# Optimization experiments

Measured on AMD Instinct MI355X. Metric: run time of the kernel, lower is better.

## Reference

```python
import jax, jax.numpy as jnp
import numpy as np

B, N, M = 2, 10000, 320000
F, LAT, STY = 64, 128, 128
HEADS, HID = 4, 32
OUT = 3 + F  # 67
NEG = 0.2    # leaky relu slope (both activation and GAT attention)
EPS = 1e-5


def leaky(x):
    return jax.nn.leaky_relu(x, NEG)


def layer_norm(x, g, b):
    mu = jnp.mean(x, axis=-1, keepdims=True)
    var = jnp.var(x, axis=-1, keepdims=True)
    return (x - mu) * jax.lax.rsqrt(var + EPS) * g + b


def gat_conv(h, src, dst, W, a_src, a_dst, bias, heads, out_dim, n_nodes, concat):
    # h: [n, in]; W: [in, heads*out_dim]; a_*: [heads, out_dim]
    ht = (h @ W).reshape(n_nodes, heads, out_dim)
    al_s = jnp.einsum('nhd,hd->nh', ht, a_src)  # source contribution
    al_d = jnp.einsum('nhd,hd->nh', ht, a_dst)  # destination contribution
    e = leaky(al_s[src] + al_d[dst])            # [E, heads]
    emax = jax.ops.segment_max(e, dst, num_segments=n_nodes)
    ex = jnp.exp(e - emax[dst])
    denom = jax.ops.segment_sum(ex, dst, num_segments=n_nodes)
    alpha = ex / (denom[dst] + 1e-16)           # scatter-softmax over in-edges
    msg = ht[src] * alpha[:, :, None]           # [E, heads, out_dim]
    agg = jax.ops.segment_sum(msg, dst, num_segments=n_nodes)
    agg = agg.reshape(n_nodes, heads * out_dim) if concat else agg.mean(axis=1)
    return agg + bias


def setup_inputs():
    key = jax.random.key(0)
    ks = jax.random.split(key, 20)
    g = lambda i, sh, s=0.05: jax.random.normal(ks[i], sh, jnp.float32) * s
    d = {}
    d['z'] = g(0, (B, LAT), 1.0)
    d['x'] = g(1, (N, F), 1.0)
    d['pos'] = g(2, (N, 3), 1.0)
    d['edge_index'] = jax.random.randint(ks[3], (2, M), 0, N)
    d['w1'] = g(4, (LAT, 256)); d['b1'] = jnp.zeros((256,), jnp.float32)
    d['w2'] = g(5, (256, 512)); d['b2'] = jnp.zeros((512,), jnp.float32)
    d['w3'] = g(6, (512, STY)); d['b3'] = jnp.zeros((STY,), jnp.float32)
    in0 = F + STY
    d['gw0'] = g(7, (in0, HEADS * HID)); d['ga0s'] = g(8, (HEADS, HID)); d['ga0d'] = g(9, (HEADS, HID)); d['gb0'] = jnp.zeros((HEADS * HID,), jnp.float32)
    in1 = HEADS * HID
    d['gw1'] = g(10, (in1, HEADS * HID)); d['ga1s'] = g(11, (HEADS, HID)); d['ga1d'] = g(12, (HEADS, HID)); d['gb1'] = jnp.zeros((HEADS * HID,), jnp.float32)
    d['gw2'] = g(13, (in1, OUT)); d['ga2s'] = g(14, (1, OUT)); d['ga2d'] = g(15, (1, OUT)); d['gb2'] = jnp.zeros((OUT,), jnp.float32)
    d['ln0_g'] = jnp.ones((in1,), jnp.float32); d['ln0_b'] = jnp.zeros((in1,), jnp.float32)
    d['ln1_g'] = jnp.ones((in1,), jnp.float32); d['ln1_b'] = jnp.zeros((in1,), jnp.float32)
    return d


def _batched_edges(edge_index):
    # replicate template edges B times with node-id offsets, then add self-loops
    ei = jnp.concatenate([edge_index + b * N for b in range(B)], axis=1)
    sl = jnp.arange(B * N, dtype=edge_index.dtype)
    src = jnp.concatenate([ei[0], sl])
    dst = jnp.concatenate([ei[1], sl])
    return src, dst


def _forward(z, x, pos, src, dst,
             w1, b1, w2, b2, w3, b3,
             gw0, ga0s, ga0d, gb0, gw1, ga1s, ga1d, gb1, gw2, ga2s, ga2d, gb2,
             ln0_g, ln0_b, ln1_g, ln1_b):
    n_tot = B * N
    # style MLP
    s = leaky(z @ w1 + b1)
    s = leaky(s @ w2 + b2)
    style = s @ w3 + b3                               # [B, STY]
    xb = jnp.tile(x, (B, 1))                          # [B*N, F]
    pb = jnp.tile(pos, (B, 1))                        # [B*N, 3]
    style_exp = jnp.repeat(style, N, axis=0)          # [B*N, STY]
    H = jnp.concatenate([xb, style_exp], axis=1)
    H = gat_conv(H, src, dst, gw0, ga0s, ga0d, gb0, HEADS, HID, n_tot, True)
    H = leaky(layer_norm(H, ln0_g, ln0_b))
    H = gat_conv(H, src, dst, gw1, ga1s, ga1d, gb1, HEADS, HID, n_tot, True)
    H = leaky(layer_norm(H, ln1_g, ln1_b))
    H_out = gat_conv(H, src, dst, gw2, ga2s, ga2d, gb2, 1, OUT, n_tot, False)
    p_new = pb + H_out[:, :3]
    f_new = xb + H_out[:, 3:]
    return f_new, p_new


def reference(z, x, pos, edge_index,
              w1, b1, w2, b2, w3, b3,
              gw0, ga0s, ga0d, gb0, gw1, ga1s, ga1d, gb1, gw2, ga2s, ga2d, gb2,
              ln0_g, ln0_b, ln1_g, ln1_b):
    src, dst = _batched_edges(edge_index)
    return _forward(z, x, pos, src, dst,
                    w1, b1, w2, b2, w3, b3,
                    gw0, ga0s, ga0d, gb0, gw1, ga1s, ga1d, gb1, gw2, ga2s, ga2d, gb2,
                    ln0_g, ln0_b, ln1_g, ln1_b)
```

## Files before the change

### kernel.cpp

```cpp
#include <hip/hip_runtime.h>
#include <hip/hip_bf16.h>

#define DEV_INLINE __device__ __forceinline__

constexpr int Nn   = 10000;
constexpr int NT   = 20000;
constexpr int Me   = 320000;
constexpr int STRIDE = 96;
constexpr float NEG = 0.2f;

typedef float  f32x4  __attribute__((ext_vector_type(4)));
typedef short  bf16x8 __attribute__((ext_vector_type(8)));

DEV_INLINE float leaky(float x){ return x >= 0.f ? x : NEG*x; }

DEV_INLINE ushort f2bf(float v){
  __hip_bfloat16 h = __float2bfloat16(v);
  return *reinterpret_cast<ushort*>(&h);
}
DEV_INLINE float bf2f(ushort u){
  uint x = ((uint)u) << 16;
  return __uint_as_float(x);
}
DEV_INLINE float sel4(float4 w, int h){
  return h < 2 ? (h == 0 ? w.x : w.y) : (h == 2 ? w.z : w.w);
}
DEV_INLINE float red16(float v){
  v += __shfl_xor(v, 1); v += __shfl_xor(v, 2);
  v += __shfl_xor(v, 4); v += __shfl_xor(v, 8);
  return v;
}
DEV_INLINE float red32(float v){
  v += __shfl_xor(v, 1); v += __shfl_xor(v, 2);
  v += __shfl_xor(v, 4); v += __shfl_xor(v, 8);
  v += __shfl_xor(v, 16);
  return v;
}

template<int K>
__global__ __launch_bounds__(256) void k_mlp(const float* __restrict__ in,
    const float* __restrict__ W, const float* __restrict__ bias,
    float* __restrict__ out, int OD, int doAct, int mlpBlocks,
    int* __restrict__ zbuf, int zn){
  if ((int)blockIdx.x >= mlpBlocks){
    int i = (blockIdx.x - mlpBlocks)*256 + threadIdx.x;
    if (i < zn) zbuf[i] = 0;
    return;
  }
  int wave = threadIdx.x >> 6, lane = threadIdx.x & 63;
  int o = blockIdx.x*4 + wave;
  if (o >= 2*OD) return;
  int b = (o >= OD) ? 1 : 0;
  int j = o - b*OD;
  const float* __restrict__ ip = in + b*K;
  float acc = 0.f;
  #pragma unroll 2
  for (int k = lane; k < K; k += 64) acc += ip[k] * W[(size_t)k*OD + j];
  #pragma unroll
  for (int off = 32; off; off >>= 1) acc += __shfl_xor(acc, off);
  if (lane == 0){
    float v = acc + (bias ? bias[j] : 0.f);
    out[o] = doAct ? leaky(v) : v;
  }
}

__global__ __launch_bounds__(256) void k_ht0(const float* __restrict__ x,
    const float* __restrict__ gw0, const float* __restrict__ styleW0,
    const float* __restrict__ a_s, const float* __restrict__ a_d,
    ushort* __restrict__ ht0, float* __restrict__ alS, float* __restrict__ alD){
  __shared__ float wl[64][128];
  __shared__ float xl[32][64];
  __shared__ float sw[2][128];
  __shared__ float stycS[2][4], stycD[2][4];
  int t = threadIdx.x;
  for (int i=t; i<64*128; i+=256) wl[i>>7][i&127] = gw0[i];
  if (t < 256) sw[t>>7][t&127] = styleW0[t];
  int row0 = blockIdx.x*32;
  for (int i=t; i<32*64; i+=256){
    int r = i>>6, c = i&63; int gr = row0 + r;
    xl[r][c] = (gr < Nn) ? x[gr*64 + c] : 0.f;
  }
  __syncthreads();
  int c = t & 127, rh = t >> 7, lane = t & 63;
  float as_c = a_s[c], ad_c = a_d[c];
  int h = c >> 5;

  if (t < 128){
    float v0s = sw[0][c]*as_c, v0d = sw[0][c]*ad_c;
    float v1s = sw[1][c]*as_c, v1d = sw[1][c]*ad_c;
    v0s = red32(v0s); v0d = red32(v0d);
    v1s = red32(v1s); v1d = red32(v1d);
    if ((lane & 31) == 0){
      stycS[0][h] = v0s; stycD[0][h] = v0d;
      stycS[1][h] = v1s; stycD[1][h] = v1d;
    }
  }

  float acc[16];
  #pragma unroll
  for (int i=0;i<16;i++) acc[i]=0.f;
  for (int k=0;k<64;k++){
    float w = wl[k][c];
    #pragma unroll
    for (int i=0;i<16;i++) acc[i] += xl[rh+2*i][k]*w;
  }
  __syncthreads();
  float s0 = sw[0][c], s1 = sw[1][c];
  #pragma unroll
  for (int i=0;i<16;i++){
    int gr = row0 + rh + 2*i;
    if (gr < Nn){
      ht0[(size_t)gr*128 + c]      = f2bf(acc[i] + s0);
      ht0[(size_t)(Nn+gr)*128 + c] = f2bf(acc[i] + s1);
    }
    float vs = acc[i]*as_c, vd = acc[i]*ad_c;
    vs = red32(vs); vd = red32(vd);
    if ((lane & 31) == 0 && gr < Nn){
      alS[(size_t)gr*4 + h]      = vs + stycS[0][h];
      alD[(size_t)gr*4 + h]      = vd + stycD[0][h];
      alS[(size_t)(Nn+gr)*4 + h] = vs + stycS[1][h];
      alD[(size_t)(Nn+gr)*4 + h] = vd + stycD[1][h];
    }
  }
}

template<int NCOL, int LDO, int NF, int NHEAD>
__global__ __launch_bounds__(256) void k_mm_mfma(const ushort* __restrict__ A,
    const float* __restrict__ W, ushort* __restrict__ out,
    const float* __restrict__ a_s, const float* __restrict__ a_d,
    float* __restrict__ alS, float* __restrict__ alD, int M){
  constexpr int NCOLP = NF*16;
  __shared__ ushort bt[NCOLP*128];
  int t = threadIdx.x;
  int wid = t >> 6, lane = t & 63, l15 = lane & 15, g = lane >> 4;
  int mbase = blockIdx.x*128 + wid*32;

  bf16x8 afr[2][4];
  #pragma unroll
  for (int mf=0; mf<2; mf++){
    int row = mbase + mf*16 + l15;
    int rc = row < M ? row : M-1;
    const ushort* ap = A + (size_t)rc*128 + g*8;
    #pragma unroll
    for (int ks=0; ks<4; ks++)
      afr[mf][ks] = *(const bf16x8*)(ap + ks*32);
  }

  for (int idx = t; idx < 128*NCOLP; idx += 256){
    int k = idx / NCOLP, c = idx % NCOLP;
    float v = (c < NCOL) ? W[k*NCOL + c] : 0.f;
    uint byte = ((uint)(c*128 + k) << 1) ^ ((uint)(c&7) << 4);
    *(ushort*)((char*)bt + byte) = f2bf(v);
  }
  __syncthreads();

  f32x4 acc[2][NF];
  #pragma unroll
  for (int mf=0; mf<2; mf++)
    #pragma unroll
    for (int nf=0; nf<NF; nf++) acc[mf][nf] = (f32x4){0.f,0.f,0.f,0.f};

  #pragma unroll
  for (int ks=0; ks<4; ks++){
    int kb = ks*32 + g*8;
    bf16x8 bfr[NF];
    #pragma unroll
    for (int nf=0; nf<NF; nf++){
      int c = nf*16 + l15;
      uint byte = ((uint)(c*128 + kb) << 1) ^ ((uint)(c&7) << 4);
      bfr[nf] = *(const bf16x8*)((const char*)bt + byte);
    }
    #pragma unroll
    for (int mf=0; mf<2; mf++)
      #pragma unroll
      for (int nf=0; nf<NF; nf++)
        acc[mf][nf] = __builtin_amdgcn_mfma_f32_16x16x32_bf16(
            afr[mf][ks], bfr[nf], acc[mf][nf], 0, 0, 0);
  }

  #pragma unroll
  for (int mf=0; mf<2; mf++){
    int rbase = mbase + mf*16 + g*4;
    #pragma unroll
    for (int nf=0; nf<NF; nf++){
      int c = nf*16 + l15;
      if (c < LDO){
        #pragma unroll
        for (int r=0; r<4; r++){
          int row = rbase + r;
          if (row < M) out[(size_t)row*LDO + c] = (c < NCOL) ? f2bf(acc[mf][nf][r]) : (ushort)0;
        }
      }
    }
  }

  float as_v[NF], ad_v[NF];
  #pragma unroll
  for (int nf=0; nf<NF; nf++){
    int c = nf*16 + l15;
    as_v[nf] = (c < NCOL) ? a_s[c] : 0.f;
    ad_v[nf] = (c < NCOL) ? a_d[c] : 0.f;
  }
  #pragma unroll
  for (int mf=0; mf<2; mf++){
    #pragma unroll
    for (int r=0; r<4; r++){
      int row = mbase + mf*16 + g*4 + r;
      if (NHEAD == 4){
        float ps0 = acc[mf][0][r]*as_v[0] + acc[mf][1][r]*as_v[1];
        float ps1 = acc[mf][2][r]*as_v[2] + acc[mf][3][r]*as_v[3];
        float ps2 = acc[mf][4][r]*as_v[4] + acc[mf][5][r]*as_v[5];
        float ps3 = acc[mf][6][r]*as_v[6] + acc[mf][7][r]*as_v[7];
        float pd0 = acc[mf][0][r]*ad_v[0] + acc[mf][1][r]*ad_v[1];
        float pd1 = acc[mf][2][r]*ad_v[2] + acc[mf][3][r]*ad_v[3];
        float pd2 = acc[mf][4][r]*ad_v[4] + acc[mf][5][r]*ad_v[5];
        float pd3 = acc[mf][6][r]*ad_v[6] + acc[mf][7][r]*ad_v[7];
        ps0 = red16(ps0); ps1 = red16(ps1); ps2 = red16(ps2); ps3 = red16(ps3);
        pd0 = red16(pd0); pd1 = red16(pd1); pd2 = red16(pd2); pd3 = red16(pd3);
        if (l15 == 0 && row < M){
          *(float4*)(alS + (size_t)row*4) = make_float4(ps0, ps1, ps2, ps3);
          *(float4*)(alD + (size_t)row*4) = make_float4(pd0, pd1, pd2, pd3);
        }
      } else {
        float ps = 0.f, pd = 0.f;
        #pragma unroll
        for (int nf=0; nf<NF; nf++){
          ps += acc[mf][nf][r]*as_v[nf];
          pd += acc[mf][nf][r]*ad_v[nf];
        }
        ps = red16(ps); pd = red16(pd);
        if (l15 == 0 && row < M){
          alS[row] = ps; alD[row] = pd;
        }
      }
    }
  }
}

__global__ void k_scatter(const int* __restrict__ eidx,
    int* __restrict__ cnt, ushort* __restrict__ slot){
  int e = blockIdx.x*256 + threadIdx.x;
  if (e >= Me) return;
  int s = eidx[e], d = eidx[Me + e];
  int p = atomicAdd(&cnt[d], 1);
  if (p < STRIDE) slot[(size_t)d*STRIDE + p] = (ushort)s;
}

__global__ __launch_bounds__(256) void k_gat128(const ushort* __restrict__ ht,
    const float* __restrict__ alS, const float* __restrict__ alD,
    const int* __restrict__ deg, const ushort* __restrict__ slot,
    const float* __restrict__ gb, const float* __restrict__ lng,
    const float* __restrict__ lnb, ushort* __restrict__ outH, int n){
  __shared__ float4 wbuf[4][64];
  __shared__ int    sbuf[4][64];
  int wave = threadIdx.x >> 6, lane = threadIdx.x & 63;
  int dd = blockIdx.x*4 + wave;
  if (dd >= n) return;
  int tr  = (dd >= Nn) ? dd - Nn : dd;
  int off = (dd >= Nn) ? Nn : 0;
  int c0 = lane*2;
  int h  = lane >> 4;
  float4 ald4 = *(const float4*)(alD + dd*4);
  int dg = deg[tr]; if (dg > STRIDE) dg = STRIDE;
  int begin = tr*STRIDE, end = begin + dg;

  float4 asl = *(const float4*)(alS + dd*4);
  float4 wsl;
  wsl.x = __expf(leaky(asl.x + ald4.x));
  wsl.y = __expf(leaky(asl.y + ald4.y));
  wsl.z = __expf(leaky(asl.z + ald4.z));
  wsl.w = __expf(leaky(asl.w + ald4.w));
  float es = sel4(wsl, h);
  uint sv0 = *(const uint*)(ht + (size_t)dd*128 + c0);
  float den  = es;
  float acc0 = es * bf2f((ushort)(sv0 & 0xffff));
  float acc1 = es * bf2f((ushort)(sv0 >> 16));

  const ushort* __restrict__ htp = ht + c0;

  for (int j = begin; j < end; j += 64){
    int nc = min(64, end - j);
    if (lane < nc){
      int s = (int)slot[j + lane] + off;
      float4 as4 = *(const float4*)(alS + s*4);
      float4 w;
      w.x = __expf(leaky(as4.x + ald4.x));
      w.y = __expf(leaky(as4.y + ald4.y));
      w.z = __expf(leaky(as4.z + ald4.z));
      w.w = __expf(leaky(as4.w + ald4.w));
      wbuf[wave][lane] = w;
      sbuf[wave][lane] = s;
    }
    int q = 0;
    for (; q + 8 <= nc; q += 8){
      int sv[8]; float4 wv[8];
      #pragma unroll
      for (int u=0;u<8;u++){ sv[u] = sbuf[wave][q+u]; wv[u] = wbuf[wave][q+u]; }
      uint hv[8];
      #pragma unroll
      for (int u=0;u<8;u++) hv[u] = *(const uint*)(htp + (size_t)sv[u]*128);
      #pragma unroll
      for (int u=0;u<8;u++){
        float e = sel4(wv[u], h);
        den  += e;
        acc0 += e * bf2f((ushort)(hv[u] & 0xffff));
        acc1 += e * bf2f((ushort)(hv[u] >> 16));
      }
    }
    for (; q < nc; q++){
      int s = sbuf[wave][q];
      float e = sel4(wbuf[wave][q], h);
      uint hv = *(const uint*)(htp + (size_t)s*128);
      den  += e;
      acc0 += e * bf2f((ushort)(hv & 0xffff));
      acc1 += e * bf2f((ushort)(hv >> 16));
    }
  }
  float idn = 1.f / (den + 1e-16f);
  float v0 = acc0*idn + gb[c0];
  float v1 = acc1*idn + gb[c0+1];

  float sum = v0 + v1, sq = v0*v0 + v1*v1;
  #pragma unroll
  for (int offx = 32; offx; offx >>= 1){
    sum += __shfl_xor(sum, offx);
    sq  += __shfl_xor(sq,  offx);
  }
  float mu  = sum * (1.f/128.f);
  float var = sq  * (1.f/128.f) - mu*mu;
  float inv = rsqrtf(var + 1e-5f);
  float y0 = (v0 - mu)*inv*lng[c0]   + lnb[c0];
  float y1 = (v1 - mu)*inv*lng[c0+1] + lnb[c0+1];
  uint ow = (uint)f2bf(leaky(y0)) | ((uint)f2bf(leaky(y1)) << 16);
  *(uint*)(outH + (size_t)dd*128 + c0) = ow;
}

__global__ __launch_bounds__(256) void k_gat_out(const ushort* __restrict__ ht2,
    const float* __restrict__ alS, const float* __restrict__ alD,
    const int* __restrict__ deg, const ushort* __restrict__ slot,
    const float* __restrict__ gb2, const float* __restrict__ x,
    const float* __restrict__ pos, float* __restrict__ out, int n){
  __shared__ float wbuf[4][64];
  __shared__ int   sbuf[4][64];
  int wave = threadIdx.x >> 6, lane = threadIdx.x & 63;
  int dd = blockIdx.x*4 + wave;
  if (dd >= n) return;
  int tr  = (dd >= Nn) ? dd - Nn : dd;
  int off = (dd >= Nn) ? Nn : 0;
  int c0 = lane*2;
  bool act = (c0 < 67);
  float ald = alD[dd];
  int dg = deg[tr]; if (dg > STRIDE) dg = STRIDE;
  int begin = tr*STRIDE, end = begin + dg;

  float wsl = __expf(leaky(alS[dd] + ald));
  float den  = wsl;
  uint sv0 = act ? *(const uint*)(ht2 + (size_t)dd*68 + c0) : 0u;
  float acc0 = wsl * bf2f((ushort)(sv0 & 0xffff));
  float acc1 = wsl * bf2f((ushort)(sv0 >> 16));

  const ushort* __restrict__ h2p = ht2 + c0;

  for (int j = begin; j < end; j += 64){
    int nc = min(64, end - j);
    if (lane < nc){
      int s = (int)slot[j + lane] + off;
      wbuf[wave][lane] = __expf(leaky(alS[s] + ald));
      sbuf[wave][lane] = s;
    }
    int q = 0;
    for (; q + 8 <= nc; q += 8){
      int sv[8]; float wv[8];
      #pragma unroll
      for (int u=0;u<8;u++){ sv[u] = sbuf[wave][q+u]; wv[u] = wbuf[wave][q+u]; }
      uint hv[8];
      #pragma unroll
      for (int u=0;u<8;u++) hv[u] = act ? *(const uint*)(h2p + (size_t)sv[u]*68) : 0u;
      #pragma unroll
      for (int u=0;u<8;u++){
        den  += wv[u];
        acc0 += wv[u] * bf2f((ushort)(hv[u] & 0xffff));
        acc1 += wv[u] * bf2f((ushort)(hv[u] >> 16));
      }
    }
    for (; q < nc; q++){
      int s = sbuf[wave][q]; float w = wbuf[wave][q];
      uint hv = act ? *(const uint*)(h2p + (size_t)s*68) : 0u;
      den  += w;
      acc0 += w * bf2f((ushort)(hv & 0xffff));
      acc1 += w * bf2f((ushort)(hv >> 16));
    }
  }
  if (!act) return;
  float idn = 1.f / (den + 1e-16f);
  int i = tr;
  int c1 = c0 + 1;
  float v0 = acc0*idn + gb2[c0];
  if (c0 < 3) out[NT*64 + dd*3 + c0] = pos[i*3 + c0] + v0;
  else        out[dd*64 + (c0-3)]    = x[i*64 + (c0-3)] + v0;
  if (c1 < 67){
    float v1 = acc1*idn + gb2[c1];
    if (c1 < 3) out[NT*64 + dd*3 + c1] = pos[i*3 + c1] + v1;
    else        out[dd*64 + (c1-3)]    = x[i*64 + (c1-3)] + v1;
  }
}

extern "C" void kernel_launch(void* const* d_in, const int* in_sizes, int n_in,
                              void* d_out, int out_size, void* d_ws, size_t ws_size,
                              hipStream_t stream){
  const float* z    = (const float*)d_in[0];
  const float* x    = (const float*)d_in[1];
  const float* pos  = (const float*)d_in[2];
  const int*   eidx = (const int*)  d_in[3];
  const float* w1   = (const float*)d_in[4];
  const float* b1   = (const float*)d_in[5];
  const float* w2   = (const float*)d_in[6];
  const float* b2   = (const float*)d_in[7];
  const float* w3   = (const float*)d_in[8];
  const float* b3   = (const float*)d_in[9];
  const float* gw0  = (const float*)d_in[10];
  const float* ga0s = (const float*)d_in[11];
  const float* ga0d = (const float*)d_in[12];
  const float* gb0  = (const float*)d_in[13];
  const float* gw1  = (const float*)d_in[14];
  const float* ga1s = (const float*)d_in[15];
  const float* ga1d = (const float*)d_in[16];
  const float* gb1  = (const float*)d_in[17];
  const float* gw2  = (const float*)d_in[18];
  const float* ga2s = (const float*)d_in[19];
  const float* ga2d = (const float*)d_in[20];
  const float* gb2  = (const float*)d_in[21];
  const float* ln0g = (const float*)d_in[22];
  const float* ln0b = (const float*)d_in[23];
  const float* ln1g = (const float*)d_in[24];
  const float* ln1b = (const float*)d_in[25];
  float* out = (float*)d_out;

  float* ws       = (float*)d_ws;
  float* styleW0  = ws;
  float* s1buf    = ws + 256;
  float* s2buf    = s1buf + 512;
  float* stbuf    = s2buf + 1024;
  float* alS      = stbuf + 256;
  float* alD      = alS + 80000;
  ushort* htA     = (ushort*)(alD + 80000);
  ushort* htB     = htA + (size_t)NT*128;
  ushort* ht2c    = htB + (size_t)NT*128;
  int*   cnt      = (int*)(ht2c + (size_t)NT*68);
  ushort* slot    = (ushort*)(cnt + Nn);

  const int ZB = (Nn + 255)/256;
  k_mlp<128><<<128 + ZB, 256, 0, stream>>>(z,     w1, b1, s1buf, 256, 1, 128, cnt, Nn);
  k_mlp<256><<<256,      256, 0, stream>>>(s1buf, w2, b2, s2buf, 512, 1, 256, nullptr, 0);
  k_mlp<512><<<64,       256, 0, stream>>>(s2buf, w3, b3, stbuf, 128, 0, 64, nullptr, 0);
  k_mlp<128><<<64,       256, 0, stream>>>(stbuf, gw0 + 64*128, (const float*)nullptr, styleW0, 128, 0, 64, nullptr, 0);

  k_scatter<<<(Me+255)/256, 256, 0, stream>>>(eidx, cnt, slot);

  const int MB = (NT+127)/128;
  k_ht0<<<(Nn+31)/32, 256, 0, stream>>>(x, gw0, styleW0, ga0s, ga0d, htA, alS, alD);
  k_gat128<<<(NT+3)/4, 256, 0, stream>>>(htA, alS, alD, cnt, slot,
                                         gb0, ln0g, ln0b, htB, NT);
  k_mm_mfma<128,128,8,4><<<MB, 256, 0, stream>>>(htB, gw1, htA, ga1s, ga1d, alS, alD, NT);
  k_gat128<<<(NT+3)/4, 256, 0, stream>>>(htA, alS, alD, cnt, slot,
                                         gb1, ln1g, ln1b, htB, NT);
  k_mm_mfma<67,68,5,1><<<MB, 256, 0, stream>>>(htB, gw2, ht2c, ga2s, ga2d, alS, alD, NT);
  k_gat_out<<<(NT+3)/4, 256, 0, stream>>>(ht2c, alS, alD, cnt, slot,
                                          gb2, x, pos, out, NT);
}
```

Baseline: 157.4 us.

## Use MFMA for first GAT projection and fuse edge scatter into its launch

The first-layer x@W projection moves from a scalar FP32 shared-memory GEMM to a bf16 MFMA kernel with a swizzled LDS weight tile. The bf16 conversion of x is folded into the first MLP launch as extra blocks. The edge-scatter kernel is merged into the same launch as the projection to save a launch. The attention weight buffer in k_gat128 changes to a per-head layout so each lane reads its own head's scalar instead of selecting from a float4. Converting x to bf16 adds rounding before the first projection.

Measured after the change: 136.7 us. 13.2% less time.

```diff
diff --git a/kernel.cpp b/kernel.cpp
--- a/kernel.cpp
+++ b/kernel.cpp
@@ -41,10 +41,22 @@
 __global__ __launch_bounds__(256) void k_mlp(const float* __restrict__ in,
     const float* __restrict__ W, const float* __restrict__ bias,
     float* __restrict__ out, int OD, int doAct, int mlpBlocks,
-    int* __restrict__ zbuf, int zn){
+    int* __restrict__ zbuf, int zn, int zblk,
+    const float* __restrict__ xsrc, ushort* __restrict__ xdst, int xn4){
   if ((int)blockIdx.x >= mlpBlocks){
-    int i = (blockIdx.x - mlpBlocks)*256 + threadIdx.x;
-    if (i < zn) zbuf[i] = 0;
+    int b2 = blockIdx.x - mlpBlocks;
+    if (b2 < zblk){
+      int i = b2*256 + threadIdx.x;
+      if (i < zn) zbuf[i] = 0;
+    } else {
+      int i4 = (b2 - zblk)*256 + threadIdx.x;
+      if (i4 < xn4){
+        float4 v = ((const float4*)xsrc)[i4];
+        ushort4 o;
+        o.x = f2bf(v.x); o.y = f2bf(v.y); o.z = f2bf(v.z); o.w = f2bf(v.w);
+        ((ushort4*)xdst)[i4] = o;
+      }
+    }
     return;
   }
   int wave = threadIdx.x >> 6, lane = threadIdx.x & 63;
@@ -64,62 +76,124 @@
   }
 }
 
-__global__ __launch_bounds__(256) void k_ht0(const float* __restrict__ x,
+__global__ __launch_bounds__(256) void k_ht0_mfma(const ushort* __restrict__ xb,
     const float* __restrict__ gw0, const float* __restrict__ styleW0,
     const float* __restrict__ a_s, const float* __restrict__ a_d,
-    ushort* __restrict__ ht0, float* __restrict__ alS, float* __restrict__ alD){
-  __shared__ float wl[64][128];
-  __shared__ float xl[32][64];
-  __shared__ float sw[2][128];
+    ushort* __restrict__ ht0, float* __restrict__ alS, float* __restrict__ alD,
+    int mbBlocks, const int* __restrict__ eidx, int* __restrict__ cnt,
+    ushort* __restrict__ slot){
+  if ((int)blockIdx.x >= mbBlocks){
+    int e = (blockIdx.x - mbBlocks)*256 + threadIdx.x;
+    if (e < Me){
+      int s = eidx[e], d = eidx[Me + e];
+      int p = atomicAdd(&cnt[d], 1);
+      if (p < STRIDE) slot[(size_t)d*STRIDE + p] = (ushort)s;
+    }
+    return;
+  }
+  __shared__ ushort bt[128*64];
   __shared__ float stycS[2][4], stycD[2][4];
   int t = threadIdx.x;
-  for (int i=t; i<64*128; i+=256) wl[i>>7][i&127] = gw0[i];
-  if (t < 256) sw[t>>7][t&127] = styleW0[t];
-  int row0 = blockIdx.x*32;
-  for (int i=t; i<32*64; i+=256){
-    int r = i>>6, c = i&63; int gr = row0 + r;
-    xl[r][c] = (gr < Nn) ? x[gr*64 + c] : 0.f;
-  }
-  __syncthreads();
-  int c = t & 127, rh = t >> 7, lane = t & 63;
-  float as_c = a_s[c], ad_c = a_d[c];
-  int h = c >> 5;
+  int wid = t >> 6, lane = t & 63, l15 = lane & 15, g = lane >> 4;
+  int mbase = blockIdx.x*128 + wid*32;
+
+  bf16x8 afr[2][2];
+  #pragma unroll
+  for (int mf=0; mf<2; mf++){
+    int row = mbase + mf*16 + l15;
+    int rc = row < Nn ? row : Nn-1;
+    const ushort* ap = xb + (size_t)rc*64 + g*8;
+    #pragma unroll
+    for (int ks=0; ks<2; ks++)
+      afr[mf][ks] = *(const bf16x8*)(ap + ks*32);
+  }
+
+  for (int idx = t; idx < 64*128; idx += 256){
+    int k = idx >> 7, c = idx & 127;
+    uint byte = ((uint)(c*64 + k) << 1) ^ ((uint)(c&7) << 4);
+    *(ushort*)((char*)bt + byte) = f2bf(gw0[k*128 + c]);
+  }
 
   if (t < 128){
-    float v0s = sw[0][c]*as_c, v0d = sw[0][c]*ad_c;
-    float v1s = sw[1][c]*as_c, v1d = sw[1][c]*ad_c;
-    v0s = red32(v0s); v0d = red32(v0d);
-    v1s = red32(v1s); v1d = red32(v1d);
+    int c = t, h = c >> 5;
+    float as_c = a_s[c], ad_c = a_d[c];
+    float s0 = styleW0[c], s1 = styleW0[128 + c];
+    float v0s = red32(s0*as_c), v0d = red32(s0*ad_c);
+    float v1s = red32(s1*as_c), v1d = red32(s1*ad_c);
     if ((lane & 31) == 0){
       stycS[0][h] = v0s; stycD[0][h] = v0d;
       stycS[1][h] = v1s; stycD[1][h] = v1d;
     }
   }
-
-  float acc[16];
-  #pragma unroll
-  for (int i=0;i<16;i++) acc[i]=0.f;
-  for (int k=0;k<64;k++){
-    float w = wl[k][c];
-    #pragma unroll
-    for (int i=0;i<16;i++) acc[i] += xl[rh+2*i][k]*w;
-  }
   __syncthreads();
-  float s0 = sw[0][c], s1 = sw[1][c];
-  #pragma unroll
-  for (int i=0;i<16;i++){
-    int gr = row0 + rh + 2*i;
-    if (gr < Nn){
-      ht0[(size_t)gr*128 + c]      = f2bf(acc[i] + s0);
-      ht0[(size_t)(Nn+gr)*128 + c] = f2bf(acc[i] + s1);
-    }
-    float vs = acc[i]*as_c, vd = acc[i]*ad_c;
-    vs = red32(vs); vd = red32(vd);
-    if ((lane & 31) == 0 && gr < Nn){
-      alS[(size_t)gr*4 + h]      = vs + stycS[0][h];
-      alD[(size_t)gr*4 + h]      = vd + stycD[0][h];
-      alS[(size_t)(Nn+gr)*4 + h] = vs + stycS[1][h];
-      alD[(size_t)(Nn+gr)*4 + h] = vd + stycD[1][h];
+
+  f32x4 acc[2][8];
+  #pragma unroll
+  for (int mf=0; mf<2; mf++)
+    #pragma unroll
+    for (int nf=0; nf<8; nf++) acc[mf][nf] = (f32x4){0.f,0.f,0.f,0.f};
+
+  #pragma unroll
+  for (int ks=0; ks<2; ks++){
+    int kb = ks*32 + g*8;
+    bf16x8 bfr[8];
+    #pragma unroll
+    for (int nf=0; nf<8; nf++){
+      int c = nf*16 + l15;
+      uint byte = ((uint)(c*64 + kb) << 1) ^ ((uint)(c&7) << 4);
+      bfr[nf] = *(const bf16x8*)((const char*)bt + byte);
+    }
+    #pragma unroll
+    for (int mf=0; mf<2; mf++)
+      #pragma unroll
+      for (int nf=0; nf<8; nf++)
+        acc[mf][nf] = __builtin_amdgcn_mfma_f32_16x16x32_bf16(
+            afr[mf][ks], bfr[nf], acc[mf][nf], 0, 0, 0);
+  }
+
+  float sw0[8], sw1[8], as_v[8], ad_v[8];
+  #pragma unroll
+  for (int nf=0; nf<8; nf++){
+    int c = nf*16 + l15;
+    sw0[nf] = styleW0[c]; sw1[nf] = styleW0[128 + c];
+    as_v[nf] = a_s[c];    ad_v[nf] = a_d[c];
+  }
+  #pragma unroll
+  for (int mf=0; mf<2; mf++){
+    int rbase = mbase + mf*16 + g*4;
+    #pragma unroll
+    for (int r=0; r<4; r++){
+      int row = rbase + r;
+      bool ok = (row < Nn);
+      #pragma unroll
+      for (int nf=0; nf<8; nf++){
+        int c = nf*16 + l15;
+        if (ok){
+          float v = acc[mf][nf][r];
+          ht0[(size_t)row*128 + c]      = f2bf(v + sw0[nf]);
+          ht0[(size_t)(Nn+row)*128 + c] = f2bf(v + sw1[nf]);
+        }
+      }
+      float ps0 = acc[mf][0][r]*as_v[0] + acc[mf][1][r]*as_v[1];
+      float ps1 = acc[mf][2][r]*as_v[2] + acc[mf][3][r]*as_v[3];
+      float ps2 = acc[mf][4][r]*as_v[4] + acc[mf][5][r]*as_v[5];
+      float ps3 = acc[mf][6][r]*as_v[6] + acc[mf][7][r]*as_v[7];
+      float pd0 = acc[mf][0][r]*ad_v[0] + acc[mf][1][r]*ad_v[1];
+      float pd1 = acc[mf][2][r]*ad_v[2] + acc[mf][3][r]*ad_v[3];
+      float pd2 = acc[mf][4][r]*ad_v[4] + acc[mf][5][r]*ad_v[5];
+      float pd3 = acc[mf][6][r]*ad_v[6] + acc[mf][7][r]*ad_v[7];
+      ps0 = red16(ps0); ps1 = red16(ps1); ps2 = red16(ps2); ps3 = red16(ps3);
+      pd0 = red16(pd0); pd1 = red16(pd1); pd2 = red16(pd2); pd3 = red16(pd3);
+      if (l15 == 0 && ok){
+        *(float4*)(alS + (size_t)row*4) = make_float4(
+            ps0 + stycS[0][0], ps1 + stycS[0][1], ps2 + stycS[0][2], ps3 + stycS[0][3]);
+        *(float4*)(alD + (size_t)row*4) = make_float4(
+            pd0 + stycD[0][0], pd1 + stycD[0][1], pd2 + stycD[0][2], pd3 + stycD[0][3]);
+        *(float4*)(alS + (size_t)(Nn+row)*4) = make_float4(
+            ps0 + stycS[1][0], ps1 + stycS[1][1], ps2 + stycS[1][2], ps3 + stycS[1][3]);
+        *(float4*)(alD + (size_t)(Nn+row)*4) = make_float4(
+            pd0 + stycD[1][0], pd1 + stycD[1][1], pd2 + stycD[1][2], pd3 + stycD[1][3]);
+      }
     }
   }
 }
@@ -237,22 +311,13 @@
   }
 }
 
-__global__ void k_scatter(const int* __restrict__ eidx,
-    int* __restrict__ cnt, ushort* __restrict__ slot){
-  int e = blockIdx.x*256 + threadIdx.x;
-  if (e >= Me) return;
-  int s = eidx[e], d = eidx[Me + e];
-  int p = atomicAdd(&cnt[d], 1);
-  if (p < STRIDE) slot[(size_t)d*STRIDE + p] = (ushort)s;
-}
-
 __global__ __launch_bounds__(256) void k_gat128(const ushort* __restrict__ ht,
     const float* __restrict__ alS, const float* __restrict__ alD,
     const int* __restrict__ deg, const ushort* __restrict__ slot,
     const float* __restrict__ gb, const float* __restrict__ lng,
     const float* __restrict__ lnb, ushort* __restrict__ outH, int n){
-  __shared__ float4 wbuf[4][64];
-  __shared__ int    sbuf[4][64];
+  __shared__ float wbuf[4][4][68];
+  __shared__ int   sbuf[4][64];
   int wave = threadIdx.x >> 6, lane = threadIdx.x & 63;
   int dd = blockIdx.x*4 + wave;
   if (dd >= n) return;
@@ -283,33 +348,31 @@
     if (lane < nc){
       int s = (int)slot[j + lane] + off;
       float4 as4 = *(const float4*)(alS + s*4);
-      float4 w;
-      w.x = __expf(leaky(as4.x + ald4.x));
-      w.y = __expf(leaky(as4.y + ald4.y));
-      w.z = __expf(leaky(as4.z + ald4.z));
-      w.w = __expf(leaky(as4.w + ald4.w));
-      wbuf[wave][lane] = w;
+      wbuf[wave][0][lane] = __expf(leaky(as4.x + ald4.x));
+      wbuf[wave][1][lane] = __expf(leaky(as4.y + ald4.y));
+      wbuf[wave][2][lane] = __expf(leaky(as4.z + ald4.z));
+      wbuf[wave][3][lane] = __expf(leaky(as4.w + ald4.w));
       sbuf[wave][lane] = s;
     }
+    const float* __restrict__ wh = wbuf[wave][h];
     int q = 0;
     for (; q + 8 <= nc; q += 8){
-      int sv[8]; float4 wv[8];
-      #pragma unroll
-      for (int u=0;u<8;u++){ sv[u] = sbuf[wave][q+u]; wv[u] = wbuf[wave][q+u]; }
+      int sv[8]; float wv[8];
+      #pragma unroll
+      for (int u=0;u<8;u++){ sv[u] = sbuf[wave][q+u]; wv[u] = wh[q+u]; }
       uint hv[8];
       #pragma unroll
       for (int u=0;u<8;u++) hv[u] = *(const uint*)(htp + (size_t)sv[u]*128);
       #pragma unroll
       for (int u=0;u<8;u++){
-        float e = sel4(wv[u], h);
-        den  += e;
-        acc0 += e * bf2f((ushort)(hv[u] & 0xffff));
-        acc1 += e * bf2f((ushort)(hv[u] >> 16));
+        den  += wv[u];
+        acc0 += wv[u] * bf2f((ushort)(hv[u] & 0xffff));
+        acc1 += wv[u] * bf2f((ushort)(hv[u] >> 16));
       }
     }
     for (; q < nc; q++){
       int s = sbuf[wave][q];
-      float e = sel4(wbuf[wave][q], h);
+      float e = wh[q];
       uint hv = *(const uint*)(htp + (size_t)s*128);
       den  += e;
       acc0 += e * bf2f((ushort)(hv & 0xffff));
@@ -446,21 +509,29 @@
   ushort* htA     = (ushort*)(alD + 80000);
   ushort* htB     = htA + (size_t)NT*128;
   ushort* ht2c    = htB + (size_t)NT*128;
-  int*   cnt      = (int*)(ht2c + (size_t)NT*68);
+  ushort* xb      = ht2c + (size_t)NT*68;
+  int*   cnt      = (int*)(xb + (size_t)Nn*64);
   ushort* slot    = (ushort*)(cnt + Nn);
 
   const int ZB = (Nn + 255)/256;
-  k_mlp<128><<<128 + ZB, 256, 0, stream>>>(z,     w1, b1, s1buf, 256, 1, 128, cnt, Nn);
-  k_mlp<256><<<256,      256, 0, stream>>>(s1buf, w2, b2, s2buf, 512, 1, 256, nullptr, 0);
-  k_mlp<512><<<64,       256, 0, stream>>>(s2buf, w3, b3, stbuf, 128, 0, 64, nullptr, 0);
-  k_mlp<128><<<64,       256, 0, stream>>>(stbuf, gw0 + 64*128, (const float*)nullptr, styleW0, 128, 0, 64, nullptr, 0);
-
-  k_scatter<<<(Me+255)/256, 256, 0, stream>>>(eidx, cnt, slot);
-
-  const int MB = (NT+127)/128;
-  k_ht0<<<(Nn+31)/32, 256, 0, stream>>>(x, gw0, styleW0, ga0s, ga0d, htA, alS, alD);
+  const int XB = (Nn*64/4 + 255)/256;
+  k_mlp<128><<<128 + ZB + XB, 256, 0, stream>>>(z, w1, b1, s1buf, 256, 1, 128,
+                                                cnt, Nn, ZB, x, xb, Nn*64/4);
+  k_mlp<256><<<256, 256, 0, stream>>>(s1buf, w2, b2, s2buf, 512, 1, 256,
+                                      nullptr, 0, 0, nullptr, nullptr, 0);
+  k_mlp<512><<<64,  256, 0, stream>>>(s2buf, w3, b3, stbuf, 128, 0, 64,
+                                      nullptr, 0, 0, nullptr, nullptr, 0);
+  k_mlp<128><<<64,  256, 0, stream>>>(stbuf, gw0 + 64*128, (const float*)nullptr,
+                                      styleW0, 128, 0, 64,
+                                      nullptr, 0, 0, nullptr, nullptr, 0);
+
+  const int MB0 = (Nn+127)/128;
+  const int EB  = (Me+255)/256;
+  k_ht0_mfma<<<MB0 + EB, 256, 0, stream>>>(xb, gw0, styleW0, ga0s, ga0d,
+                                           htA, alS, alD, MB0, eidx, cnt, slot);
   k_gat128<<<(NT+3)/4, 256, 0, stream>>>(htA, alS, alD, cnt, slot,
                                          gb0, ln0g, ln0b, htB, NT);
+  const int MB = (NT+127)/128;
   k_mm_mfma<128,128,8,4><<<MB, 256, 0, stream>>>(htB, gw1, htA, ga1s, ga1d, alS, alD, NT);
   k_gat128<<<(NT+3)/4, 256, 0, stream>>>(htA, alS, alD, cnt, slot,
                                          gb1, ln1g, ln1b, htB, NT);
```
